# Performance work log

Hardware: AMD Instinct MI355X
Metric: run time of the kernel (lower is better)

Reference implementation:

```python
import jax, jax.numpy as jnp
import numpy as np

NUM_HEADS = 8
WINDOW = 33  # must be odd for seq length to be preserved


def setup_inputs() -> dict:
    key = jax.random.key(0)
    ks = jax.random.split(key, 7)
    B, S, E = 4, 2048, 256
    sc = 1.0 / np.sqrt(E)
    return {
        "x": jax.random.normal(ks[0], (B, S, E), dtype=jnp.float32),
        "Wq": jax.random.normal(ks[1], (E, E), dtype=jnp.float32) * sc,
        "bq": jax.random.normal(ks[2], (E,), dtype=jnp.float32) * 0.01,
        "Wk": jax.random.normal(ks[3], (E, E), dtype=jnp.float32) * sc,
        "bk": jax.random.normal(ks[4], (E,), dtype=jnp.float32) * 0.01,
        "Wv": jax.random.normal(ks[5], (E, E), dtype=jnp.float32) * sc,
        "bv": jax.random.normal(ks[6], (E,), dtype=jnp.float32) * 0.01,
    }


def reference(x, Wq, bq, Wk, bk, Wv, bv):
    B, S, E = x.shape
    H = NUM_HEADS
    D = E // H
    W = WINDOW
    pad = (W - 1) // 2
    scale = D ** (-0.5)

    def heads(t):  # [B,S,E] -> [B,H,S,D]
        return t.reshape(B, S, H, D).transpose(0, 2, 1, 3)

    q = heads(x @ Wq + bq)
    k = heads(x @ Wk + bk)
    v = heads(x @ Wv + bv)

    K = S - W + 1  # number of k/v windows (unfold with step=1)
    kv_idx = jnp.arange(K)[:, None] + jnp.arange(W)[None, :]  # [K,W]
    k_unf = k[:, :, kv_idx, :]  # [B,H,K,W,D]
    v_unf = v[:, :, kv_idx, :]  # [B,H,K,W,D]

    q_pad = jnp.pad(q, ((0, 0), (0, 0), (pad, pad), (0, 0)))  # zero pad seq
    q_idx = jnp.arange(S)[:, None] + jnp.arange(W)[None, :]  # [S,W]
    q_unf = q_pad[:, :, q_idx, :]  # [B,H,S,W,D]

    # contract over BOTH window and head dim (faithful to the torch einsums)
    scores = jnp.einsum('bhqwd,bhkwd->bhqk', q_unf, k_unf) * scale  # [B,H,S,K]
    attn = jax.nn.softmax(scores, axis=-1)
    out = jnp.einsum('bhqk,bhkwd->bhqd', attn, v_unf)  # sums v over window too
    return out.transpose(0, 2, 1, 3).reshape(B, S, E)
```

## Files before the change

### kernel.cpp

```cpp
#include <hip/hip_runtime.h>
#include <hip/hip_bf16.h>
#include <math.h>

#define BB   4
#define SS   2048
#define EE   256
#define HH   8
#define DD   32
#define WW   33
#define KKN  (SS - WW + 1)
#define SCALE 0.17677669529663687f
#define FMAX 20.0f
#define SCALE2 0.25503486f
#define FM2    28.853900817779268f

typedef __attribute__((ext_vector_type(8))) short short8v;
typedef __attribute__((ext_vector_type(4))) short short4v;
typedef __attribute__((ext_vector_type(4))) float float4v;

__device__ __forceinline__ short f2bf(float f) {
    union { __hip_bfloat16 h; short s; } c;
    c.h = __float2bfloat16(f);
    return c.s;
}

__device__ __forceinline__ short2 f2bf2(float a, float b) {
    union { __hip_bfloat162 h; short2 s; } c;
    float2 f; f.x = a; f.y = b;
    c.h = __float22bfloat162_rn(f);
    return c.s;
}

#if __has_builtin(__builtin_amdgcn_exp2f)
__device__ __forceinline__ float exp2_fast(float x) { return __builtin_amdgcn_exp2f(x); }
#else
__device__ __forceinline__ float exp2_fast(float x) { return __expf(x * 0.6931471805599453f); }
#endif

__global__ __launch_bounds__(256) void qkv_kernel(
    const float* __restrict__ x,
    const float* __restrict__ Wq, const float* __restrict__ bq,
    const float* __restrict__ Wk, const float* __restrict__ bk,
    const float* __restrict__ Wv, const float* __restrict__ bv,
    short* __restrict__ qo, short* __restrict__ ko, float* __restrict__ vo)
{
    __shared__ alignas(16) float xs[64][68];
    __shared__ alignas(16) float ws[64][68];

    const int t   = threadIdx.x;
    const int r0  = blockIdx.x * 64;
    const int ct  = blockIdx.y;
    const int mat = ct >> 2;
    const int cm0 = (ct & 3) * 64;
    const float* Wm   = (mat == 0) ? Wq : (mat == 1) ? Wk : Wv;
    const float* bias = (mat == 0) ? bq : (mat == 1) ? bk : bv;

    const int tr = t >> 4, tc = t & 15;

    float acc[4][4];
#pragma unroll
    for (int i = 0; i < 4; i++)
#pragma unroll
        for (int j = 0; j < 4; j++) acc[i][j] = 0.f;

    for (int ec = 0; ec < 4; ec++) {
        const int e0 = ec * 64;
        __syncthreads();
#pragma unroll
        for (int i = 0; i < 4; i++) {
            int L = t + i * 256;
            int r = L >> 4, c4 = (L & 15) * 4;
            *(float4*)&xs[r][c4] = *(const float4*)(x  + (size_t)(r0 + r) * EE + e0 + c4);
            *(float4*)&ws[r][c4] = *(const float4*)(Wm + (size_t)(e0 + r) * EE + cm0 + c4);
        }
        __syncthreads();

#pragma unroll
        for (int eg = 0; eg < 16; eg++) {
            float4 xv[4], wv4[4];
#pragma unroll
            for (int i = 0; i < 4; i++) xv[i]  = *(const float4*)&xs[tr * 4 + i][eg * 4];
#pragma unroll
            for (int j = 0; j < 4; j++) wv4[j] = *(const float4*)&ws[eg * 4 + j][tc * 4];
            const float* w0p = (const float*)&wv4[0];
            const float* w1p = (const float*)&wv4[1];
            const float* w2p = (const float*)&wv4[2];
            const float* w3p = (const float*)&wv4[3];
#pragma unroll
            for (int i = 0; i < 4; i++)
#pragma unroll
                for (int j = 0; j < 4; j++)
                    acc[i][j] = acc[i][j] + xv[i].x * w0p[j] + xv[i].y * w1p[j]
                                          + xv[i].z * w2p[j] + xv[i].w * w3p[j];
        }
    }

    const int cmb = cm0 + tc * 4;
    const int h = cmb >> 5, d0 = cmb & 31;
    float b4[4];
#pragma unroll
    for (int j = 0; j < 4; j++) b4[j] = bias[cmb + j];

#pragma unroll
    for (int i = 0; i < 4; i++) {
        int row = r0 + tr * 4 + i;
        int b_  = row >> 11;
        int s   = row & 2047;
        size_t o = (((size_t)(b_ * HH + h)) * SS + s) * DD + d0;
        if (mat == 2) {
            float4 vv;
            vv.x = acc[i][0] + b4[0]; vv.y = acc[i][1] + b4[1];
            vv.z = acc[i][2] + b4[2]; vv.w = acc[i][3] + b4[3];
            *(float4*)(vo + o) = vv;
        } else {
            short4v sv;
            sv.x = f2bf(acc[i][0] + b4[0]); sv.y = f2bf(acc[i][1] + b4[1]);
            sv.z = f2bf(acc[i][2] + b4[2]); sv.w = f2bf(acc[i][3] + b4[3]);
            *(short4v*)(((mat == 0) ? qo : ko) + o) = sv;
        }
    }
}

__global__ __launch_bounds__(64) void vs_kernel(
    const float* __restrict__ v, short* __restrict__ vsT)
{
    const int t   = threadIdx.x;
    const int d4  = t & 7;
    const int kkb = blockIdx.x * 8 + (t >> 3);
    const int bh  = blockIdx.y;
    if (kkb >= 252) return;
    const int kb0 = kkb * 8;

    const float4* vp = (const float4*)(v + ((size_t)bh * SS + kb0) * DD) + d4;
    float4 rbuf[7];
    float4 acc = {0.f, 0.f, 0.f, 0.f};
#pragma unroll
    for (int w = 0; w < WW; w++) {
        float4 xv = vp[w * 8];
        if (w < 7) rbuf[w] = xv;
        acc.x += xv.x; acc.y += xv.y; acc.z += xv.z; acc.w += xv.w;
    }
    short8v sh[4];
    sh[0][0] = f2bf(acc.x); sh[1][0] = f2bf(acc.y);
    sh[2][0] = f2bf(acc.z); sh[3][0] = f2bf(acc.w);
#pragma unroll
    for (int s = 1; s < 8; s++) {
        float4 sub = rbuf[s - 1];
        float4 add = vp[(s + 32) * 8];
        acc.x += add.x - sub.x; acc.y += add.y - sub.y;
        acc.z += add.z - sub.z; acc.w += add.w - sub.w;
        sh[0][s] = f2bf(acc.x); sh[1][s] = f2bf(acc.y);
        sh[2][s] = f2bf(acc.z); sh[3][s] = f2bf(acc.w);
    }
#pragma unroll
    for (int j = 0; j < 4; j++) {
        short* op = vsT + ((size_t)bh * DD + 4 * d4 + j) * KKN + kb0;
        *(short8v*)op = sh[j];
    }
}

__global__ __launch_bounds__(256, 4) void attn_kernel(
    const short* __restrict__ qg, const short* __restrict__ kg,
    const short* __restrict__ vsTg, float* __restrict__ out)
{
    __shared__ alignas(16) short QbS[64][40];
    __shared__ alignas(16) short Kb[96][40];
    __shared__ alignas(16) short Gst[96][72];
    __shared__ alignas(16) short vT[32][72];
    __shared__ float lrow[32];

    short (*Qb)[40] = QbS;
    short (*pb)[72] = (short (*)[72])QbS;

    const int t  = threadIdx.x;
    const int qt = blockIdx.x;
    const int bh = blockIdx.y;
    const int q0 = qt * 32;

    const short* qb   = qg   + (size_t)bh * SS * DD;
    const short* kb   = kg   + (size_t)bh * SS * DD;
    const short* vsTb = vsTg + (size_t)bh * DD * KKN;

    const int lane = t & 63, wv = t >> 6;
    const int quad = lane >> 4, lr = lane & 15;
    const int ptm = wv >> 1, ptn = wv & 1;
    const int jcol = 64 + (t & 7);

    const int qitw  = wv & 1;
    const int tbase = wv >> 1;
    const int qi    = qitw * 16 + lr;

    const int vd  = t >> 3, vc8 = (t & 7) * 8;
    const int r2  = t >> 2, c8r = (t & 3) * 8;

    {
        short8v z = {0, 0, 0, 0, 0, 0, 0, 0};
        short* g = &Gst[0][0];
        for (int i = t; i < 864; i += 256) *(short8v*)(g + 8 * i) = z;
    }

    {
        int gq = q0 - 16 + r2;
        if (gq >= 0 && gq < SS) {
            *(short8v*)&Qb[r2][c8r] = *(const short8v*)(qb + (size_t)gq * DD + c8r);
        } else {
            float4 z = {0.f, 0.f, 0.f, 0.f};
            *(float4*)&Qb[r2][c8r] = z;
        }
        *(short8v*)&Kb[r2][c8r] = *(const short8v*)(kb + (size_t)r2 * DD + c8r);
        if (t < 128)
            *(short8v*)&Kb[64 + r2][c8r] = *(const short8v*)(kb + (size_t)(64 + r2) * DD + c8r);
    }
    if (t < 32) lrow[t] = 0.f;
    __syncthreads();

    short8v Qf[4];
#pragma unroll
    for (int tq = 0; tq < 4; tq++)
        Qf[tq] = *(const short8v*)&Qb[tq * 16 + lr][quad * 8];

    short8v Ufw[2];
#pragma unroll
    for (int ch = 0; ch < 2; ch++) {
        short8v u;
#pragma unroll
        for (int j = 0; j < 8; j++) {
            int m = ch * 32 + quad * 8 + j;
            u[j] = (qi <= m && m <= qi + 32) ? (short)0x3F80 : (short)0;
        }
        Ufw[ch] = u;
    }

    float4v acc = {0.f, 0.f, 0.f, 0.f};
    float lsumw = 0.f;
    const int npass = (wv < 2) ? 2 : 1;
    int k0m = 0;

    for (int kt = 0; kt < 32; kt++) {
        const int k0 = kt * 64;
        for (int pass = 0; pass < npass; pass++) {
            const int tk = wv + pass * 4;
            int krow = k0m + tk * 16 + lr; if (krow >= 96) krow -= 96;
            const short8v A = *(const short8v*)&Kb[krow][quad * 8];
#pragma unroll
            for (int tq = 0; tq < 4; tq++) {
                const int del = tk - tq;
                if (del < -2 || del > 4) continue;
                float4v c0 = {0.f, 0.f, 0.f, 0.f};
                c0 = __builtin_amdgcn_mfma_f32_16x16x32_bf16(A, Qf[tq], c0, 0, 0, 0);
                const int i   = tq * 16 + lr;
                const int j2b = tk * 16 + quad * 4 - i + 31;
                short* gbase = &Gst[0][i];
                short2 g01 = f2bf2(c0[0], c0[1]);
                short2 g23 = f2bf2(c0[2], c0[3]);
                short gv[4] = {g01.x, g01.y, g23.x, g23.y};
#pragma unroll
                for (int e = 0; e < 4; e++) {
                    int j2 = j2b + e;
                    short* dst = ((unsigned)j2 < 95u) ? (gbase + j2 * 72)
                                                      : (gbase + 95 * 72);
                    *dst = gv[e];
                }
            }
        }

        if (kt > 0) {
            const short8v Ap0 = *(const short8v*)&pb[ptm * 16 + lr][quad * 8];
            const short8v Ap1 = *(const short8v*)&pb[ptm * 16 + lr][32 + quad * 8];
            const short8v Bv0 = *(const short8v*)&vT[ptn * 16 + lr][quad * 8];
            const short8v Bv1 = *(const short8v*)&vT[ptn * 16 + lr][32 + quad * 8];
            __builtin_amdgcn_s_setprio(1);
            acc = __builtin_amdgcn_mfma_f32_16x16x32_bf16(Ap0, Bv0, acc, 0, 0, 0);
            acc = __builtin_amdgcn_mfma_f32_16x16x32_bf16(Ap1, Bv1, acc, 0, 0, 0);
            __builtin_amdgcn_s_setprio(0);
        }
        __syncthreads();

        {
            int col = k0 + vc8; if (col > KKN - 8) col = KKN - 8;
            *(short8v*)&vT[vd][vc8] = *(const short8v*)(vsTb + (size_t)vd * KKN + col);
        }
        if (kt < 31) {
            int gp = k0 + 96 + r2;
            int ga = (gp < SS) ? gp : (SS - 1);
            int slot = k0m + r2; if (slot >= 96) slot -= 96;
            *(short8v*)&Kb[slot][c8r] = *(const short8v*)(kb + (size_t)ga * DD + c8r);
        }

        const unsigned lim = (kt == 31) ? 32u : 64u;
        if (kt == 31) {
            short4v z4 = {0, 0, 0, 0};
            int zr = t >> 3, zc = (t & 7) * 4 + 32;
            *(short4v*)&pb[zr][zc] = z4;
        }

        short* prow = &pb[qi][0];
#pragma unroll
        for (int u = 0; u < 3; u++) {
            const int tile = 2 * u + tbase;
            const int jrow = tile * 16 + lr;
            const short8v A0f = *(const short8v*)&Gst[jrow][quad * 8];
            const short8v A1f = *(const short8v*)&Gst[jrow][32 + quad * 8];
            float4v D = {0.f, 0.f, 0.f, 0.f};
            __builtin_amdgcn_s_setprio(1);
            D = __builtin_amdgcn_mfma_f32_16x16x32_bf16(A0f, Ufw[0], D, 0, 0, 0);
            D = __builtin_amdgcn_mfma_f32_16x16x32_bf16(A1f, Ufw[1], D, 0, 0, 0);
            __builtin_amdgcn_s_setprio(0);
            const int kib = qi + tile * 16 + quad * 4 - 31;
            float p0 = exp2_fast(fmaf(D[0], SCALE2, -FM2));
            float p1 = exp2_fast(fmaf(D[1], SCALE2, -FM2));
            float p2 = exp2_fast(fmaf(D[2], SCALE2, -FM2));
            float p3 = exp2_fast(fmaf(D[3], SCALE2, -FM2));
            short2 c01 = f2bf2(p0, p1);
            short2 c23 = f2bf2(p2, p3);
            float pv[4] = {p0, p1, p2, p3};
            short cv[4] = {c01.x, c01.y, c23.x, c23.y};
#pragma unroll
            for (int e = 0; e < 4; e++) {
                int ki = kib + e;
                bool ok = (unsigned)ki < lim;
                short* dst = ok ? (prow + ki) : (prow + jcol);
                *dst = cv[e];
                lsumw += ok ? pv[e] : 0.f;
            }
        }
        __syncthreads();
        k0m += 64; if (k0m >= 96) k0m -= 96;
    }

    {
        const short8v Ap0 = *(const short8v*)&pb[ptm * 16 + lr][quad * 8];
        const short8v Ap1 = *(const short8v*)&pb[ptm * 16 + lr][32 + quad * 8];
        const short8v Bv0 = *(const short8v*)&vT[ptn * 16 + lr][quad * 8];
        const short8v Bv1 = *(const short8v*)&vT[ptn * 16 + lr][32 + quad * 8];
        acc = __builtin_amdgcn_mfma_f32_16x16x32_bf16(Ap0, Bv0, acc, 0, 0, 0);
        acc = __builtin_amdgcn_mfma_f32_16x16x32_bf16(Ap1, Bv1, acc, 0, 0, 0);
    }

    {
        float s = lsumw;
        s += __shfl_xor(s, 16);
        s += __shfl_xor(s, 32);
        if (quad == 0) atomicAdd(&lrow[qitw * 16 + lr], s);
    }
    __syncthreads();

    {
        const int rrow = ptm * 16 + quad * 4;
        const int col  = ptn * 16 + lr;
        const int b_ = bh >> 3, h = bh & 7;
#pragma unroll
        for (int e = 0; e < 4; e++) {
            int s_ = q0 + rrow + e;
            out[((size_t)(b_ * SS + s_)) * EE + h * DD + col] = acc[e] / lrow[rrow + e];
        }
    }
}

extern "C" void kernel_launch(void* const* d_in, const int* in_sizes, int n_in,
                              void* d_out, int out_size, void* d_ws, size_t ws_size,
                              hipStream_t stream)
{
    (void)in_sizes; (void)n_in; (void)out_size; (void)ws_size;
    const float* x  = (const float*)d_in[0];
    const float* Wq = (const float*)d_in[1];
    const float* bq = (const float*)d_in[2];
    const float* Wk = (const float*)d_in[3];
    const float* bk = (const float*)d_in[4];
    const float* Wv = (const float*)d_in[5];
    const float* bv = (const float*)d_in[6];
    float* out = (float*)d_out;

    const size_t REG = (size_t)BB * HH * SS * DD;
    short* qbf   = (short*)d_ws;
    short* kbf   = qbf + REG;
    float* vbuf  = (float*)(kbf + REG);
    short* vsTb  = (short*)(vbuf + REG);

    qkv_kernel<<<dim3(128, 12), dim3(256), 0, stream>>>(x, Wq, bq, Wk, bk, Wv, bv,
                                                        qbf, kbf, vbuf);
    vs_kernel<<<dim3(32, 32), dim3(64), 0, stream>>>(vbuf, vsTb);
    attn_kernel<<<dim3(64, 32), dim3(256), 0, stream>>>(qbf, kbf, vsTb, out);
}
```

Before: 275.8 us.

## Compute Q/K projections with split-bf16 MFMA instead of fp32 SIMT GEMM

```diff
diff --git a/kernel.cpp b/kernel.cpp
--- a/kernel.cpp
+++ b/kernel.cpp
@@ -24,6 +24,12 @@
     return c.s;
 }
 
+__device__ __forceinline__ float bf2f(short h) {
+    union { unsigned u; float f; } c;
+    c.u = ((unsigned)(unsigned short)h) << 16;
+    return c.f;
+}
+
 __device__ __forceinline__ short2 f2bf2(float a, float b) {
     union { __hip_bfloat162 h; short2 s; } c;
     float2 f; f.x = a; f.y = b;
@@ -37,19 +43,133 @@
 __device__ __forceinline__ float exp2_fast(float x) { return __expf(x * 0.6931471805599453f); }
 #endif
 
+__global__ __launch_bounds__(256) void cvt_kernel(
+    const float* __restrict__ x,
+    const float* __restrict__ Wq, const float* __restrict__ Wk,
+    short* __restrict__ xh, short* __restrict__ xl,
+    short* __restrict__ wth, short* __restrict__ wtl)
+{
+    const int t  = threadIdx.x;
+    const int bx = blockIdx.x;
+    if (bx < 1024) {
+        size_t i8 = ((size_t)bx * 256 + t) * 8;
+        float4 f0 = *(const float4*)(x + i8);
+        float4 f1 = *(const float4*)(x + i8 + 4);
+        float f[8] = {f0.x, f0.y, f0.z, f0.w, f1.x, f1.y, f1.z, f1.w};
+        short8v h, l;
+#pragma unroll
+        for (int j = 0; j < 8; j++) {
+            short hb = f2bf(f[j]);
+            h[j] = hb;
+            l[j] = f2bf(f[j] - bf2f(hb));
+        }
+        *(short8v*)(xh + i8) = h;
+        *(short8v*)(xl + i8) = l;
+    } else {
+        int o   = (bx - 1024) * 2048 + t * 8;
+        int mat = o >> 16;
+        int rem = o & 65535;
+        int n = rem >> 8, k0 = rem & 255;
+        const float* W = mat ? Wk : Wq;
+        short8v h, l;
+#pragma unroll
+        for (int j = 0; j < 8; j++) {
+            float f = W[(size_t)(k0 + j) * 256 + n];
+            short hb = f2bf(f);
+            h[j] = hb;
+            l[j] = f2bf(f - bf2f(hb));
+        }
+        *(short8v*)(wth + o) = h;
+        *(short8v*)(wtl + o) = l;
+    }
+}
+
+__global__ __launch_bounds__(256) void qk_mfma_kernel(
+    const short* __restrict__ xh, const short* __restrict__ xl,
+    const short* __restrict__ wth, const short* __restrict__ wtl,
+    const float* __restrict__ bq, const float* __restrict__ bk,
+    short* __restrict__ qo, short* __restrict__ ko)
+{
+    __shared__ alignas(16) short xsh[64][40];
+    __shared__ alignas(16) short xsl[64][40];
+    __shared__ alignas(16) short wsh[128][40];
+    __shared__ alignas(16) short wsl[128][40];
+
+    const int t   = threadIdx.x;
+    const int r0  = blockIdx.x * 64;
+    const int mat = blockIdx.y >> 1;
+    const int cb  = blockIdx.y & 1;
+    const int lane = t & 63, wv = t >> 6;
+    const int quad = lane >> 4, lr = lane & 15;
+    const float* bias = mat ? bk : bq;
+    short* op = mat ? ko : qo;
+    const size_t wofs = (size_t)(mat * 256 + cb * 128) * 256;
+    const short* wthm = wth + wofs;
+    const short* wtlm = wtl + wofs;
+
+    float4v acc[8];
+#pragma unroll
+    for (int ct = 0; ct < 8; ct++) acc[ct] = (float4v){0.f, 0.f, 0.f, 0.f};
+
+    for (int kk = 0; kk < 8; kk++) {
+        __syncthreads();
+        {
+            int r = t >> 2, c8 = (t & 3) * 8;
+            size_t go = (size_t)(r0 + r) * 256 + kk * 32 + c8;
+            *(short8v*)&xsh[r][c8] = *(const short8v*)(xh + go);
+            *(short8v*)&xsl[r][c8] = *(const short8v*)(xl + go);
+        }
+#pragma unroll
+        for (int i = 0; i < 2; i++) {
+            int L = t + i * 256;
+            int wr = L >> 2, c8 = (L & 3) * 8;
+            size_t go = (size_t)wr * 256 + kk * 32 + c8;
+            *(short8v*)&wsh[wr][c8] = *(const short8v*)(wthm + go);
+            *(short8v*)&wsl[wr][c8] = *(const short8v*)(wtlm + go);
+        }
+        __syncthreads();
+
+        const short8v ah = *(const short8v*)&xsh[wv * 16 + lr][quad * 8];
+        const short8v al = *(const short8v*)&xsl[wv * 16 + lr][quad * 8];
+#pragma unroll
+        for (int ct = 0; ct < 8; ct++) {
+            const short8v bh_ = *(const short8v*)&wsh[ct * 16 + lr][quad * 8];
+            const short8v bl_ = *(const short8v*)&wsl[ct * 16 + lr][quad * 8];
+            acc[ct] = __builtin_amdgcn_mfma_f32_16x16x32_bf16(ah, bh_, acc[ct], 0, 0, 0);
+            acc[ct] = __builtin_amdgcn_mfma_f32_16x16x32_bf16(ah, bl_, acc[ct], 0, 0, 0);
+            acc[ct] = __builtin_amdgcn_mfma_f32_16x16x32_bf16(al, bh_, acc[ct], 0, 0, 0);
+        }
+    }
+
+#pragma unroll
+    for (int ct = 0; ct < 8; ct++) {
+        int col = cb * 128 + ct * 16 + lr;
+        float bv_ = bias[col];
+        int h = col >> 5, d = col & 31;
+#pragma unroll
+        for (int e = 0; e < 4; e++) {
+            int row = r0 + wv * 16 + quad * 4 + e;
+            int b_ = row >> 11, s = row & 2047;
+            size_t o = (((size_t)(b_ * HH + h)) * SS + s) * DD + d;
+            op[o] = f2bf(acc[ct][e] + bv_);
+        }
+    }
+}
+
 __global__ __launch_bounds__(256) void qkv_kernel(
     const float* __restrict__ x,
     const float* __restrict__ Wq, const float* __restrict__ bq,
     const float* __restrict__ Wk, const float* __restrict__ bk,
     const float* __restrict__ Wv, const float* __restrict__ bv,
-    short* __restrict__ qo, short* __restrict__ ko, float* __restrict__ vo)
+    short* __restrict__ qo, short* __restrict__ ko, float* __restrict__ vo,
+    int ct0)
 {
     __shared__ alignas(16) float xs[64][68];
     __shared__ alignas(16) float ws[64][68];
 
     const int t   = threadIdx.x;
     const int r0  = blockIdx.x * 64;
-    const int ct  = blockIdx.y;
+    const int ct  = blockIdx.y + ct0;
     const int mat = ct >> 2;
     const int cm0 = (ct & 3) * 64;
     const float* Wm   = (mat == 0) ? Wq : (mat == 1) ? Wk : Wv;
@@ -377,8 +497,16 @@
     float* vbuf  = (float*)(kbf + REG);
     short* vsTb  = (short*)(vbuf + REG);
 
-    qkv_kernel<<<dim3(128, 12), dim3(256), 0, stream>>>(x, Wq, bq, Wk, bk, Wv, bv,
-                                                        qbf, kbf, vbuf);
+    short* xh  = (short*)vbuf;
+    short* xl  = xh + REG;
+    short* wth = (short*)out;
+    short* wtl = wth + 2 * 256 * 256;
+
+    cvt_kernel<<<dim3(1088), dim3(256), 0, stream>>>(x, Wq, Wk, xh, xl, wth, wtl);
+    qk_mfma_kernel<<<dim3(128, 4), dim3(256), 0, stream>>>(xh, xl, wth, wtl,
+                                                           bq, bk, qbf, kbf);
+    qkv_kernel<<<dim3(128, 4), dim3(256), 0, stream>>>(x, Wq, bq, Wk, bk, Wv, bv,
+                                                       qbf, kbf, vbuf, 8);
     vs_kernel<<<dim3(32, 32), dim3(64), 0, stream>>>(vbuf, vsTb);
     attn_kernel<<<dim3(64, 32), dim3(256), 0, stream>>>(qbf, kbf, vsTb, out);
 }
```

Result: faster. 262.7 us (-4.8%).
